# Kernel optimization log

Measured on AMD Instinct MI355X. Metric: run time of the kernel, lower is better.

The kernel has to match this reference:

```python
import jax, jax.numpy as jnp
import numpy as np

N_NODES = 100000
N_EDGES = 1000000
H = 128  # hidden_size


def setup_inputs() -> dict:
    key = jax.random.key(0)
    ks = jax.random.split(key, 8)
    emb = jax.random.normal(ks[0], (N_NODES, H), dtype=jnp.float32)
    edge_index = jax.random.randint(ks[1], (2, N_EDGES), 0, N_NODES, dtype=jnp.int64)
    # MLP([2H, 4H, H, 1]) weights (Kaiming-ish scaled normals)
    W1 = jax.random.normal(ks[2], (2 * H, 4 * H), dtype=jnp.float32) / np.sqrt(2 * H).astype(np.float32)
    b1 = jnp.zeros((4 * H,), dtype=jnp.float32)
    W2 = jax.random.normal(ks[3], (4 * H, H), dtype=jnp.float32) / np.sqrt(4 * H).astype(np.float32)
    b2 = jnp.zeros((H,), dtype=jnp.float32)
    W3 = jax.random.normal(ks[4], (H, 1), dtype=jnp.float32) / np.sqrt(H).astype(np.float32)
    b3 = jnp.zeros((1,), dtype=jnp.float32)
    return {"emb": emb, "edge_index": edge_index,
            "W1": W1, "b1": b1, "W2": W2, "b2": b2, "W3": W3, "b3": b3}


def reference(emb, edge_index, W1, b1, W2, b2, W3, b3):
    # ExtractorMLP.forward with learn_edge_att=True, eval mode.
    col = edge_index[0]
    row = edge_index[1]
    # edge-gather + concat: [E, 2H]
    f12 = jnp.concatenate([emb[col], emb[row]], axis=-1)
    # MLP([2H, 4H, H, 1]); Dropout is identity in eval mode
    h = jax.nn.relu(f12 @ W1 + b1)          # [E, 4H]
    h = jax.nn.relu(h @ W2 + b2)            # [E, H]
    att_log_logits = h @ W3 + b3            # [E, 1]
    # concrete_sample with training=False -> plain sigmoid
    att = jax.nn.sigmoid(att_log_logits)
    return att
```

## Files before the change

### kernel.cpp

```cpp
#include <hip/hip_runtime.h>
#include <math.h>

#define E_TOTAL   1000000
#define HDIM      128
#define K1        256
#define N1        512
#define N2        128
#define M_TILE    64
#define BLOCK     256

typedef _Float16 f16;
typedef _Float16 f16_4  __attribute__((ext_vector_type(4)));
typedef _Float16 f16_8  __attribute__((ext_vector_type(8)));
typedef float    f32_16 __attribute__((ext_vector_type(16)));

__global__ void prep_weights(const float* __restrict__ W1, const float* __restrict__ W2,
                             f16* __restrict__ W1F, f16* __restrict__ W2F) {
    int t = blockIdx.x * blockDim.x + threadIdx.x;
    const int total1 = K1 * N1;
    const int total2 = N1 * N2;
    if (t < total1) {
        int v    = t & 7;
        int lane = (t >> 3) & 63;
        int kc   = (t >> 9) & 15;
        int nt   = t >> 13;
        int k = kc * 16 + (lane >> 5) * 8 + v;
        int n = nt * 32 + (lane & 31);
        W1F[t] = (f16)W1[k * N1 + n];
    } else if (t < total1 + total2) {
        int u = t - total1;
        int v    = u & 7;
        int lane = (u >> 3) & 63;
        int kcg  = (u >> 9) & 31;
        int nt   = u >> 14;
        int k = kcg * 16 + (lane >> 5) * 8 + v;
        int n = nt * 32 + (lane & 31);
        W2F[u] = (f16)W2[k * N2 + n];
    }
}

__global__ void prep_emb(const float* __restrict__ emb, f16* __restrict__ emb16) {
    int t = blockIdx.x * blockDim.x + threadIdx.x;
    float4 f = ((const float4*)emb)[t];
    f16_4 v = { (f16)f.x, (f16)f.y, (f16)f.z, (f16)f.w };
    ((f16_4*)emb16)[t] = v;
}

template <bool F16EMB>
__global__ __launch_bounds__(BLOCK, 2) void edge_mlp_kernel(
    const float* __restrict__ emb,
    const f16*   __restrict__ emb16,
    const int*   __restrict__ eidx,
    const f16*   __restrict__ W1F,
    const float* __restrict__ b1,
    const f16*   __restrict__ W2F,
    const float* __restrict__ b2,
    const float* __restrict__ W3,
    const float* __restrict__ b3,
    float* __restrict__ out)
{
    __shared__ __align__(16) f16 sAF[2 * 16 * 64 * 8];
    __shared__ __align__(16) f16 sBF[2 * 8 * 64 * 8];
    f16* sH2F = sAF;

    const int tid = threadIdx.x;
    const int e0  = blockIdx.x * M_TILE;

    {
        const int m    = tid >> 2;
        const int side = (tid >> 1) & 1;
        const int sub  = tid & 1;
        const int met  = m >> 5;
        const int m31  = m & 31;
        const int node = eidx[side * E_TOTAL + e0 + m];
        if (F16EMB) {
            const f16* src = emb16 + (size_t)node * HDIM;
            #pragma unroll
            for (int j = 0; j < 4; ++j) {
                const int g    = side * 8 + sub * 4 + j;
                const int koff = (sub * 4 + j) * 16;
                const int psi  = side * 4 + sub * 2 + (j & 1);
                #pragma unroll
                for (int lh = 0; lh < 2; ++lh) {
                    f16_8 v = *(const f16_8*)(src + koff + lh * 8);
                    *(f16_8*)(sAF + (((met * 16 + g) * 64 + ((lh * 32 + m31) ^ psi)) << 3)) = v;
                }
            }
        } else {
            const float* src = emb + (size_t)node * HDIM;
            #pragma unroll
            for (int j = 0; j < 4; ++j) {
                const int g    = side * 8 + sub * 4 + j;
                const int koff = (sub * 4 + j) * 16;
                const int psi  = side * 4 + sub * 2 + (j & 1);
                #pragma unroll
                for (int lh = 0; lh < 2; ++lh) {
                    float4 fa = *(const float4*)(src + koff + lh * 8);
                    float4 fb = *(const float4*)(src + koff + lh * 8 + 4);
                    f16_8 v = { (f16)fa.x, (f16)fa.y, (f16)fa.z, (f16)fa.w,
                                (f16)fb.x, (f16)fb.y, (f16)fb.z, (f16)fb.w };
                    *(f16_8*)(sAF + (((met * 16 + g) * 64 + ((lh * 32 + m31) ^ psi)) << 3)) = v;
                }
            }
        }
    }
    __syncthreads();
    __builtin_amdgcn_sched_barrier(0);

    const int wnt  = tid >> 6;
    const int lane = tid & 63;
    const int l31  = lane & 31;
    const int lh   = lane >> 5;

    f16_8 ef[2][16];
    #pragma unroll
    for (int et = 0; et < 2; ++et) {
        #pragma unroll
        for (int kc = 0; kc < 16; ++kc) {
            const int psi = ((kc >> 3) & 1) * 4 + ((kc >> 2) & 1) * 2 + (kc & 1);
            const unsigned aoff =
                (unsigned)(size_t)(sAF + (((et * 16 + kc) * 64 + (lane ^ psi)) << 3));
            asm volatile("ds_read_b128 %0, %1" : "=v"(ef[et][kc]) : "v"(aoff));
        }
    }
    asm volatile("s_waitcnt lgkmcnt(0)" ::: "memory");
    __builtin_amdgcn_sched_barrier(0);

    f32_16 acc2[2] = {{0.f}, {0.f}};

    {
        f32_16 acc1[2] = {{0.f}, {0.f}};
        const int nt = wnt;
        #pragma unroll
        for (int kc = 0; kc < 16; ++kc) {
            f16_8 wf = *(const f16_8*)(W1F + (((nt * 16 + kc) * 64 + lane) << 3));
            #pragma unroll
            for (int et = 0; et < 2; ++et)
                acc1[et] = __builtin_amdgcn_mfma_f32_32x32x16_f16(wf, ef[et][kc], acc1[et], 0, 0, 0);
        }
        #pragma unroll
        for (int et = 0; et < 2; ++et) {
            #pragma unroll
            for (int g = 0; g < 4; ++g) {
                const int wnl = wnt * 32 + lh * 4 + g * 8;
                const float4 bv = *(const float4*)(b1 + wnl);
                f16_4 hv;
                #pragma unroll
                for (int i = 0; i < 4; ++i) {
                    float v = acc1[et][g * 4 + i] + ((const float*)&bv)[i];
                    hv[i] = (f16)(v > 0.f ? v : 0.f);
                }
                const int kl = wnt * 2 + (g >> 1);
                *(f16_4*)(sBF + ((((et * 8 + kl) * 64 + (g & 1) * 32 + l31) << 3) + lh * 4)) = hv;
            }
        }
    }
    __syncthreads();

    #pragma unroll
    for (int q = 1; q < 4; ++q) {
        f32_16 acc1[2] = {{0.f}, {0.f}};
        const int nt = q * 4 + wnt;
        #pragma unroll
        for (int kc = 0; kc < 16; ++kc) {
            f16_8 wf = *(const f16_8*)(W1F + (((nt * 16 + kc) * 64 + lane) << 3));
            #pragma unroll
            for (int et = 0; et < 2; ++et)
                acc1[et] = __builtin_amdgcn_mfma_f32_32x32x16_f16(wf, ef[et][kc], acc1[et], 0, 0, 0);
            if (kc < 8) {
                const int kcg = (q - 1) * 8 + kc;
                f16_8 wf2 = *(const f16_8*)(W2F + (((wnt * 32 + kcg) * 64 + lane) << 3));
                #pragma unroll
                for (int et = 0; et < 2; ++et) {
                    f16_8 ef2 = *(const f16_8*)(sBF + (((et * 8 + kc) * 64 + lane) << 3));
                    acc2[et] = __builtin_amdgcn_mfma_f32_32x32x16_f16(wf2, ef2, acc2[et], 0, 0, 0);
                }
            }
        }
        __syncthreads();
        #pragma unroll
        for (int et = 0; et < 2; ++et) {
            #pragma unroll
            for (int g = 0; g < 4; ++g) {
                const int wnl = wnt * 32 + lh * 4 + g * 8;
                const float4 bv = *(const float4*)(b1 + q * 128 + wnl);
                f16_4 hv;
                #pragma unroll
                for (int i = 0; i < 4; ++i) {
                    float v = acc1[et][g * 4 + i] + ((const float*)&bv)[i];
                    hv[i] = (f16)(v > 0.f ? v : 0.f);
                }
                const int kl = wnt * 2 + (g >> 1);
                *(f16_4*)(sBF + ((((et * 8 + kl) * 64 + (g & 1) * 32 + l31) << 3) + lh * 4)) = hv;
            }
        }
        __syncthreads();
    }

    {
        #pragma unroll
        for (int kc = 0; kc < 8; ++kc) {
            const int kcg = 24 + kc;
            f16_8 wf2 = *(const f16_8*)(W2F + (((wnt * 32 + kcg) * 64 + lane) << 3));
            #pragma unroll
            for (int et = 0; et < 2; ++et) {
                f16_8 ef2 = *(const f16_8*)(sBF + (((et * 8 + kc) * 64 + lane) << 3));
                acc2[et] = __builtin_amdgcn_mfma_f32_32x32x16_f16(wf2, ef2, acc2[et], 0, 0, 0);
            }
        }
    }

    {
        #pragma unroll
        for (int et = 0; et < 2; ++et) {
            #pragma unroll
            for (int g = 0; g < 4; ++g) {
                const int wn = wnt * 32 + lh * 4 + g * 8;
                const float4 bv = *(const float4*)(b2 + wn);
                f16_4 hv;
                #pragma unroll
                for (int i = 0; i < 4; ++i) {
                    float v = acc2[et][g * 4 + i] + ((const float*)&bv)[i];
                    hv[i] = (f16)(v > 0.f ? v : 0.f);
                }
                const int kl = wnt * 2 + (g >> 1);
                *(f16_4*)(sH2F + ((((et * 8 + kl) * 64 + (g & 1) * 32 + l31) << 3) + lh * 4)) = hv;
            }
        }
    }
    __syncthreads();

    {
        const int m   = tid >> 2;
        const int j   = tid & 3;
        const int met = m >> 5;
        const int m31 = m & 31;
        float s = 0.f;
        #pragma unroll
        for (int jj = 0; jj < 2; ++jj) {
            const int kl = j * 2 + jj;
            f16_8 a = *(const f16_8*)(sH2F + (((met * 8 + kl) * 64 + m31) << 3));
            f16_8 b = *(const f16_8*)(sH2F + (((met * 8 + kl) * 64 + 32 + m31) << 3));
            const float4* w3v = (const float4*)(W3 + kl * 16);
            float4 w0 = w3v[0], w1 = w3v[1], w2 = w3v[2], w3q = w3v[3];
            s += (float)a[0]*w0.x + (float)a[1]*w0.y + (float)a[2]*w0.z + (float)a[3]*w0.w;
            s += (float)a[4]*w1.x + (float)a[5]*w1.y + (float)a[6]*w1.z + (float)a[7]*w1.w;
            s += (float)b[0]*w2.x + (float)b[1]*w2.y + (float)b[2]*w2.z + (float)b[3]*w2.w;
            s += (float)b[4]*w3q.x + (float)b[5]*w3q.y + (float)b[6]*w3q.z + (float)b[7]*w3q.w;
        }
        s += __shfl_xor(s, 1);
        s += __shfl_xor(s, 2);
        if (j == 0) {
            const float logit = s + b3[0];
            out[e0 + m] = 1.0f / (1.0f + __expf(-logit));
        }
    }
}

extern "C" void kernel_launch(void* const* d_in, const int* in_sizes, int n_in,
                              void* d_out, int out_size, void* d_ws, size_t ws_size,
                              hipStream_t stream) {
    const float* emb  = (const float*)d_in[0];
    const int*   eidx = (const int*)d_in[1];
    const float* W1   = (const float*)d_in[2];
    const float* b1   = (const float*)d_in[3];
    const float* W2   = (const float*)d_in[4];
    const float* b2   = (const float*)d_in[5];
    const float* W3   = (const float*)d_in[6];
    const float* b3   = (const float*)d_in[7];
    float* out = (float*)d_out;

    const size_t wbytes   = (size_t)(K1 * N1 + N1 * N2) * sizeof(f16);
    const size_t embbytes = (size_t)100000 * HDIM * sizeof(f16);

    f16* W1F = (f16*)d_ws;
    f16* W2F = W1F + K1 * N1;

    const int prep_total = K1 * N1 + N1 * N2;
    prep_weights<<<(prep_total + 255) / 256, 256, 0, stream>>>(W1, W2, W1F, W2F);

    if (ws_size >= wbytes + embbytes) {
        f16* emb16 = W2F + N1 * N2;
        const int cvt_threads = 100000 * HDIM / 4;
        prep_emb<<<cvt_threads / 256, 256, 0, stream>>>(emb, emb16);
        edge_mlp_kernel<true><<<E_TOTAL / M_TILE, BLOCK, 0, stream>>>(
            emb, emb16, eidx, W1F, b1, W2F, b2, W3, b3, out);
    } else {
        edge_mlp_kernel<false><<<E_TOTAL / M_TILE, BLOCK, 0, stream>>>(
            emb, (const f16*)nullptr, eidx, W1F, b1, W2F, b2, W3, b3, out);
    }
}
```

Measured before the change: 563.0 us.

## Split warps by edge tile to halve register-held A fragments and raise occupancy

Warps are remapped so each one owns a single 32-edge tile and two output column tiles, where before each warp owned both edge tiles and one column tile. This halves the per-thread A-fragment registers (16 instead of 32 f16_8 vectors), and launch bounds are raised from 2 to 3 blocks per SIMD to exploit the lower register pressure. The cost is that each warp now loads twice as many W1/W2 weight fragments from global memory per MFMA pair, which adds L2/cache traffic.

```diff
diff --git a/kernel.cpp b/kernel.cpp
--- a/kernel.cpp
+++ b/kernel.cpp
@@ -47,7 +47,7 @@
 }
 
 template <bool F16EMB>
-__global__ __launch_bounds__(BLOCK, 2) void edge_mlp_kernel(
+__global__ __launch_bounds__(BLOCK, 3) void edge_mlp_kernel(
     const float* __restrict__ emb,
     const f16*   __restrict__ emb16,
     const int*   __restrict__ eidx,
@@ -81,9 +81,9 @@
                 const int koff = (sub * 4 + j) * 16;
                 const int psi  = side * 4 + sub * 2 + (j & 1);
                 #pragma unroll
-                for (int lh = 0; lh < 2; ++lh) {
-                    f16_8 v = *(const f16_8*)(src + koff + lh * 8);
-                    *(f16_8*)(sAF + (((met * 16 + g) * 64 + ((lh * 32 + m31) ^ psi)) << 3)) = v;
+                for (int lhp = 0; lhp < 2; ++lhp) {
+                    f16_8 v = *(const f16_8*)(src + koff + lhp * 8);
+                    *(f16_8*)(sAF + (((met * 16 + g) * 64 + ((lhp * 32 + m31) ^ psi)) << 3)) = v;
                 }
             }
         } else {
@@ -94,12 +94,12 @@
                 const int koff = (sub * 4 + j) * 16;
                 const int psi  = side * 4 + sub * 2 + (j & 1);
                 #pragma unroll
-                for (int lh = 0; lh < 2; ++lh) {
-                    float4 fa = *(const float4*)(src + koff + lh * 8);
-                    float4 fb = *(const float4*)(src + koff + lh * 8 + 4);
+                for (int lhp = 0; lhp < 2; ++lhp) {
+                    float4 fa = *(const float4*)(src + koff + lhp * 8);
+                    float4 fb = *(const float4*)(src + koff + lhp * 8 + 4);
                     f16_8 v = { (f16)fa.x, (f16)fa.y, (f16)fa.z, (f16)fa.w,
                                 (f16)fb.x, (f16)fb.y, (f16)fb.z, (f16)fb.w };
-                    *(f16_8*)(sAF + (((met * 16 + g) * 64 + ((lh * 32 + m31) ^ psi)) << 3)) = v;
+                    *(f16_8*)(sAF + (((met * 16 + g) * 64 + ((lhp * 32 + m31) ^ psi)) << 3)) = v;
                 }
             }
         }
@@ -107,21 +107,20 @@
     __syncthreads();
     __builtin_amdgcn_sched_barrier(0);
 
-    const int wnt  = tid >> 6;
+    const int w    = tid >> 6;
     const int lane = tid & 63;
     const int l31  = lane & 31;
     const int lh   = lane >> 5;
-
-    f16_8 ef[2][16];
+    const int et   = w & 1;
+    const int sg   = w >> 1;
+
+    f16_8 ef[16];
     #pragma unroll
-    for (int et = 0; et < 2; ++et) {
-        #pragma unroll
-        for (int kc = 0; kc < 16; ++kc) {
-            const int psi = ((kc >> 3) & 1) * 4 + ((kc >> 2) & 1) * 2 + (kc & 1);
-            const unsigned aoff =
-                (unsigned)(size_t)(sAF + (((et * 16 + kc) * 64 + (lane ^ psi)) << 3));
-            asm volatile("ds_read_b128 %0, %1" : "=v"(ef[et][kc]) : "v"(aoff));
-        }
+    for (int kc = 0; kc < 16; ++kc) {
+        const int psi = ((kc >> 3) & 1) * 4 + ((kc >> 2) & 1) * 2 + (kc & 1);
+        const unsigned aoff =
+            (unsigned)(size_t)(sAF + (((et * 16 + kc) * 64 + (lane ^ psi)) << 3));
+        asm volatile("ds_read_b128 %0, %1" : "=v"(ef[kc]) : "v"(aoff));
     }
     asm volatile("s_waitcnt lgkmcnt(0)" ::: "memory");
     __builtin_amdgcn_sched_barrier(0);
@@ -130,27 +129,28 @@
 
     {
         f32_16 acc1[2] = {{0.f}, {0.f}};
-        const int nt = wnt;
         #pragma unroll
         for (int kc = 0; kc < 16; ++kc) {
-            f16_8 wf = *(const f16_8*)(W1F + (((nt * 16 + kc) * 64 + lane) << 3));
-            #pragma unroll
-            for (int et = 0; et < 2; ++et)
-                acc1[et] = __builtin_amdgcn_mfma_f32_32x32x16_f16(wf, ef[et][kc], acc1[et], 0, 0, 0);
-        }
-        #pragma unroll
-        for (int et = 0; et < 2; ++et) {
+            #pragma unroll
+            for (int sp = 0; sp < 2; ++sp) {
+                const int nt = sg * 2 + sp;
+                f16_8 wf = *(const f16_8*)(W1F + (((nt * 16 + kc) * 64 + lane) << 3));
+                acc1[sp] = __builtin_amdgcn_mfma_f32_32x32x16_f16(wf, ef[kc], acc1[sp], 0, 0, 0);
+            }
+        }
+        #pragma unroll
+        for (int sp = 0; sp < 2; ++sp) {
+            const int ls = sg * 2 + sp;
             #pragma unroll
             for (int g = 0; g < 4; ++g) {
-                const int wnl = wnt * 32 + lh * 4 + g * 8;
-                const float4 bv = *(const float4*)(b1 + wnl);
+                const float4 bv = *(const float4*)(b1 + ls * 32 + g * 8 + lh * 4);
                 f16_4 hv;
                 #pragma unroll
                 for (int i = 0; i < 4; ++i) {
-                    float v = acc1[et][g * 4 + i] + ((const float*)&bv)[i];
+                    float v = acc1[sp][g * 4 + i] + ((const float*)&bv)[i];
                     hv[i] = (f16)(v > 0.f ? v : 0.f);
                 }
-                const int kl = wnt * 2 + (g >> 1);
+                const int kl = ls * 2 + (g >> 1);
                 *(f16_4*)(sBF + ((((et * 8 + kl) * 64 + (g & 1) * 32 + l31) << 3) + lh * 4)) = hv;
             }
         }
@@ -160,37 +160,38 @@
     #pragma unroll
     for (int q = 1; q < 4; ++q) {
         f32_16 acc1[2] = {{0.f}, {0.f}};
-        const int nt = q * 4 + wnt;
         #pragma unroll
         for (int kc = 0; kc < 16; ++kc) {
-            f16_8 wf = *(const f16_8*)(W1F + (((nt * 16 + kc) * 64 + lane) << 3));
-            #pragma unroll
-            for (int et = 0; et < 2; ++et)
-                acc1[et] = __builtin_amdgcn_mfma_f32_32x32x16_f16(wf, ef[et][kc], acc1[et], 0, 0, 0);
+            #pragma unroll
+            for (int sp = 0; sp < 2; ++sp) {
+                const int nt = q * 4 + sg * 2 + sp;
+                f16_8 wf = *(const f16_8*)(W1F + (((nt * 16 + kc) * 64 + lane) << 3));
+                acc1[sp] = __builtin_amdgcn_mfma_f32_32x32x16_f16(wf, ef[kc], acc1[sp], 0, 0, 0);
+            }
             if (kc < 8) {
                 const int kcg = (q - 1) * 8 + kc;
-                f16_8 wf2 = *(const f16_8*)(W2F + (((wnt * 32 + kcg) * 64 + lane) << 3));
-                #pragma unroll
-                for (int et = 0; et < 2; ++et) {
-                    f16_8 ef2 = *(const f16_8*)(sBF + (((et * 8 + kc) * 64 + lane) << 3));
-                    acc2[et] = __builtin_amdgcn_mfma_f32_32x32x16_f16(wf2, ef2, acc2[et], 0, 0, 0);
+                f16_8 ef2 = *(const f16_8*)(sBF + (((et * 8 + kc) * 64 + lane) << 3));
+                #pragma unroll
+                for (int sp2 = 0; sp2 < 2; ++sp2) {
+                    f16_8 wf2 = *(const f16_8*)(W2F + ((((sg * 2 + sp2) * 32 + kcg) * 64 + lane) << 3));
+                    acc2[sp2] = __builtin_amdgcn_mfma_f32_32x32x16_f16(wf2, ef2, acc2[sp2], 0, 0, 0);
                 }
             }
         }
         __syncthreads();
         #pragma unroll
-        for (int et = 0; et < 2; ++et) {
+        for (int sp = 0; sp < 2; ++sp) {
+            const int ls = sg * 2 + sp;
             #pragma unroll
             for (int g = 0; g < 4; ++g) {
-                const int wnl = wnt * 32 + lh * 4 + g * 8;
-                const float4 bv = *(const float4*)(b1 + q * 128 + wnl);
+                const float4 bv = *(const float4*)(b1 + q * 128 + ls * 32 + g * 8 + lh * 4);
                 f16_4 hv;
                 #pragma unroll
                 for (int i = 0; i < 4; ++i) {
-                    float v = acc1[et][g * 4 + i] + ((const float*)&bv)[i];
+                    float v = acc1[sp][g * 4 + i] + ((const float*)&bv)[i];
                     hv[i] = (f16)(v > 0.f ? v : 0.f);
                 }
-                const int kl = wnt * 2 + (g >> 1);
+                const int kl = ls * 2 + (g >> 1);
                 *(f16_4*)(sBF + ((((et * 8 + kl) * 64 + (g & 1) * 32 + l31) << 3) + lh * 4)) = hv;
             }
         }
@@ -201,29 +202,29 @@
         #pragma unroll
         for (int kc = 0; kc < 8; ++kc) {
             const int kcg = 24 + kc;
-            f16_8 wf2 = *(const f16_8*)(W2F + (((wnt * 32 + kcg) * 64 + lane) << 3));
-            #pragma unroll
-            for (int et = 0; et < 2; ++et) {
-                f16_8 ef2 = *(const f16_8*)(sBF + (((et * 8 + kc) * 64 + lane) << 3));
-                acc2[et] = __builtin_amdgcn_mfma_f32_32x32x16_f16(wf2, ef2, acc2[et], 0, 0, 0);
-            }
-        }
-    }
-
-    {
-        #pragma unroll
-        for (int et = 0; et < 2; ++et) {
+            f16_8 ef2 = *(const f16_8*)(sBF + (((et * 8 + kc) * 64 + lane) << 3));
+            #pragma unroll
+            for (int sp2 = 0; sp2 < 2; ++sp2) {
+                f16_8 wf2 = *(const f16_8*)(W2F + ((((sg * 2 + sp2) * 32 + kcg) * 64 + lane) << 3));
+                acc2[sp2] = __builtin_amdgcn_mfma_f32_32x32x16_f16(wf2, ef2, acc2[sp2], 0, 0, 0);
+            }
+        }
+    }
+
+    {
+        #pragma unroll
+        for (int sp2 = 0; sp2 < 2; ++sp2) {
+            const int s2 = sg * 2 + sp2;
             #pragma unroll
             for (int g = 0; g < 4; ++g) {
-                const int wn = wnt * 32 + lh * 4 + g * 8;
-                const float4 bv = *(const float4*)(b2 + wn);
+                const float4 bv = *(const float4*)(b2 + s2 * 32 + g * 8 + lh * 4);
                 f16_4 hv;
                 #pragma unroll
                 for (int i = 0; i < 4; ++i) {
-                    float v = acc2[et][g * 4 + i] + ((const float*)&bv)[i];
+                    float v = acc2[sp2][g * 4 + i] + ((const float*)&bv)[i];
                     hv[i] = (f16)(v > 0.f ? v : 0.f);
                 }
-                const int kl = wnt * 2 + (g >> 1);
+                const int kl = s2 * 2 + (g >> 1);
                 *(f16_4*)(sH2F + ((((et * 8 + kl) * 64 + (g & 1) * 32 + l31) << 3) + lh * 4)) = hv;
             }
         }
```

Result: slower. 1.269 ms (+125.3%).
